# Optimization experiments

Hardware: AMD Instinct MI355X
Metric: run time of the kernel (lower is better)

## Reference

```python
import jax, jax.numpy as jnp
import numpy as np

DIM = 768
NUM_HEADS = 12
HIDDEN = int(DIM * 4.0)
EPS = 1e-5


def setup_inputs() -> dict:
    key = jax.random.key(0)
    ks = jax.random.split(key, 8)
    s = lambda k, shape, scale=0.02: jax.random.normal(k, shape, dtype=jnp.float32) * scale
    return {
        "x": jax.random.normal(ks[0], (8, 1024, DIM), dtype=jnp.float32),
        "ln1_g": jnp.ones((DIM,), jnp.float32),
        "ln1_b": jnp.zeros((DIM,), jnp.float32),
        "qkv_w": s(ks[1], (DIM, 3 * DIM)),
        "qkv_b": jnp.zeros((3 * DIM,), jnp.float32),
        "proj_w": s(ks[2], (DIM, DIM)),
        "proj_b": jnp.zeros((DIM,), jnp.float32),
        "ln2_g": jnp.ones((DIM,), jnp.float32),
        "ln2_b": jnp.zeros((DIM,), jnp.float32),
        "fc1_w": s(ks[3], (DIM, HIDDEN)),
        "fc1_b": jnp.zeros((HIDDEN,), jnp.float32),
        "fc2_w": s(ks[4], (HIDDEN, DIM)),
        "fc2_b": jnp.zeros((DIM,), jnp.float32),
    }


def layer_norm(x, g, b):
    mu = jnp.mean(x, axis=-1, keepdims=True)
    var = jnp.mean(jnp.square(x - mu), axis=-1, keepdims=True)
    return (x - mu) * jax.lax.rsqrt(var + EPS) * g + b


def reference(x, ln1_g, ln1_b, qkv_w, qkv_b, proj_w, proj_b,
              ln2_g, ln2_b, fc1_w, fc1_b, fc2_w, fc2_b):
    B, N, C = x.shape
    H = NUM_HEADS
    Dh = C // H
    scale = Dh ** -0.5

    # --- Attention (pre-norm) ---
    h = layer_norm(x, ln1_g, ln1_b)
    qkv = h @ qkv_w + qkv_b                       # [B, N, 3C]
    qkv = qkv.reshape(B, N, 3, H, Dh)
    q, k, v = qkv[:, :, 0], qkv[:, :, 1], qkv[:, :, 2]  # [B, N, H, Dh]
    attn = jnp.einsum("bqhd,bkhd->bhqk", q, k) * scale  # [B, H, N, N]
    attn = jax.nn.softmax(attn, axis=-1)
    o = jnp.einsum("bhqk,bkhd->bqhd", attn, v).reshape(B, N, C)
    x = x + (o @ proj_w + proj_b)

    # --- MLP (pre-norm) ---
    h = layer_norm(x, ln2_g, ln2_b)
    h = jax.nn.gelu(h @ fc1_w + fc1_b, approximate=False)  # torch nn.GELU = exact erf
    x = x + (h @ fc2_w + fc2_b)
    return x
```

## Files before the change

kernel.cpp:

```cpp
#include <hip/hip_runtime.h>
#include <hip/hip_bf16.h>
#include <cstdint>

using f32x4  = __attribute__((ext_vector_type(4))) float;
using bf16x8 = __attribute__((ext_vector_type(8))) short;

__device__ inline ushort f2bf(float f) {
    union { float f; uint u; } x; x.f = f;
    uint u = x.u;
    return (ushort)((u + 0x7FFFu + ((u >> 16) & 1u)) >> 16);
}

__device__ inline void unpack8(uint4 v, float* out) {
    uint ws[4] = {v.x, v.y, v.z, v.w};
#pragma unroll
    for (int i = 0; i < 4; ++i) {
        union { uint u; float f; } lo, hi;
        lo.u = ws[i] << 16;
        hi.u = ws[i] & 0xFFFF0000u;
        out[2 * i]     = lo.f;
        out[2 * i + 1] = hi.f;
    }
}

__device__ inline void gload16(const ushort* g, ushort* lds) {
    __builtin_amdgcn_global_load_lds(
        (const __attribute__((address_space(1))) unsigned int*)g,
        (__attribute__((address_space(3))) unsigned int*)lds, 16, 0, 0);
}

__global__ __launch_bounds__(256) void transpose_cast(const float* __restrict__ w,
                                                      ushort* __restrict__ wt,
                                                      int K, int N) {
    __shared__ float tile[32][33];
    const int bn = blockIdx.x * 32;
    const int bk = blockIdx.y * 32;
    const int tx = threadIdx.x & 31, ty = threadIdx.x >> 5;
#pragma unroll
    for (int i = 0; i < 32; i += 8)
        tile[ty + i][tx] = w[(size_t)(bk + ty + i) * N + bn + tx];
    __syncthreads();
#pragma unroll
    for (int i = 0; i < 32; i += 8)
        wt[(size_t)(bn + ty + i) * K + bk + tx] = f2bf(tile[tx][ty + i]);
}

__global__ __launch_bounds__(256) void ln_bf16(const float* __restrict__ x,
                                               const float* __restrict__ g,
                                               const float* __restrict__ b,
                                               ushort* __restrict__ out) {
    const int row = blockIdx.x;
    const float* xr = x + (size_t)row * 768;
    const int t = threadIdx.x;
    float v0 = xr[t], v1 = xr[t + 256], v2 = xr[t + 512];
    float s  = v0 + v1 + v2;
    float sq = v0 * v0 + v1 * v1 + v2 * v2;
#pragma unroll
    for (int off = 32; off > 0; off >>= 1) {
        s  += __shfl_down(s, off);
        sq += __shfl_down(sq, off);
    }
    __shared__ float sa[4], sb[4];
    const int wv = t >> 6, lane = t & 63;
    if (lane == 0) { sa[wv] = s; sb[wv] = sq; }
    __syncthreads();
    s  = sa[0] + sa[1] + sa[2] + sa[3];
    sq = sb[0] + sb[1] + sb[2] + sb[3];
    const float mu   = s * (1.0f / 768.0f);
    const float var  = sq * (1.0f / 768.0f) - mu * mu;
    const float rstd = rsqrtf(var + 1e-5f);
    ushort* orow = out + (size_t)row * 768;
    orow[t]       = f2bf((v0 - mu) * rstd * g[t]       + b[t]);
    orow[t + 256] = f2bf((v1 - mu) * rstd * g[t + 256] + b[t + 256]);
    orow[t + 512] = f2bf((v2 - mu) * rstd * g[t + 512] + b[t + 512]);
}

template <int EPI>
__global__ __launch_bounds__(256) void gemm_bt(const ushort* __restrict__ A,
                                               const ushort* __restrict__ Bt,
                                               const float* __restrict__ bias,
                                               const float* __restrict__ resid,
                                               void* __restrict__ out,
                                               int M, int N, int K) {
    __shared__ ushort As[128 * 32];
    __shared__ ushort Bs[128 * 32];
    const int t    = threadIdx.x;
    const int lane = t & 63;
    const int w    = t >> 6;
    const int wr   = w >> 1, wc = w & 1;
    const int bm   = blockIdx.y * 128, bn = blockIdx.x * 128;
    const int lr   = lane >> 4, lc = lane & 15;
    const int srow = lane >> 2;
    const int sk8  = (lane & 3) * 8;

    const f32x4 fzero = {0.f, 0.f, 0.f, 0.f};
    f32x4 acc[4][4];
#pragma unroll
    for (int ai = 0; ai < 4; ++ai)
#pragma unroll
        for (int bj = 0; bj < 4; ++bj) acc[ai][bj] = fzero;

    const ushort* Ag0 = A  + (size_t)(bm + w * 16 + srow) * K + sk8;
    const ushort* Ag1 = Ag0 + (size_t)64 * K;
    const ushort* Bg0 = Bt + (size_t)(bn + w * 16 + srow) * K + sk8;
    const ushort* Bg1 = Bg0 + (size_t)64 * K;
    ushort* lA0 = &As[(w * 16) * 32];
    ushort* lA1 = &As[(64 + w * 16) * 32];
    ushort* lB0 = &Bs[(w * 16) * 32];
    ushort* lB1 = &Bs[(64 + w * 16) * 32];

    for (int kb = 0; kb < K; kb += 32) {
        __syncthreads();
        gload16(Ag0 + kb, lA0);
        gload16(Ag1 + kb, lA1);
        gload16(Bg0 + kb, lB0);
        gload16(Bg1 + kb, lB1);
        __syncthreads();
        bf16x8 af[4], bf[4];
#pragma unroll
        for (int ai = 0; ai < 4; ++ai)
            af[ai] = *(const bf16x8*)&As[(wr * 64 + ai * 16 + lc) * 32 + lr * 8];
#pragma unroll
        for (int bj = 0; bj < 4; ++bj)
            bf[bj] = *(const bf16x8*)&Bs[(wc * 64 + bj * 16 + lc) * 32 + lr * 8];
#pragma unroll
        for (int ai = 0; ai < 4; ++ai)
#pragma unroll
            for (int bj = 0; bj < 4; ++bj)
                acc[ai][bj] = __builtin_amdgcn_mfma_f32_16x16x32_bf16(af[ai], bf[bj],
                                                                      acc[ai][bj], 0, 0, 0);
    }

#pragma unroll
    for (int ai = 0; ai < 4; ++ai) {
#pragma unroll
        for (int bj = 0; bj < 4; ++bj) {
            int col  = bn + wc * 64 + bj * 16 + lc;
            float bs = bias[col];
#pragma unroll
            for (int j = 0; j < 4; ++j) {
                int row   = bm + wr * 64 + ai * 16 + lr * 4 + j;
                float val = acc[ai][bj][j] + bs;
                if (EPI == 1) {
                    val += resid[(size_t)row * N + col];
                    ((float*)out)[(size_t)row * N + col] = val;
                } else if (EPI == 2) {
                    val = 0.5f * val * (1.0f + erff(val * 0.70710678118f));
                    ((ushort*)out)[(size_t)row * N + col] = f2bf(val);
                } else {
                    ((ushort*)out)[(size_t)row * N + col] = f2bf(val);
                }
            }
        }
    }
}

__global__ __launch_bounds__(256) void attn_mfma(const ushort* __restrict__ qkv,
                                                 ushort* __restrict__ outb) {
    __shared__ ushort Kls[64 * 72];
    __shared__ ushort Vtls[64 * 72];
    __shared__ ushort Pls[4][32 * 72];

    const int bid = blockIdx.x;
    const int b   = bid / 96;
    const int rem = bid % 96;
    const int h   = rem >> 3;
    const int qc  = rem & 7;
    const int t    = threadIdx.x;
    const int w    = t >> 6;
    const int lane = t & 63;
    const int lr   = lane >> 4, lc = lane & 15;
    const int q0   = qc * 128 + w * 32;
    const size_t bbase = (size_t)b * 1024;

    bf16x8 qa[2][2];
#pragma unroll
    for (int rt = 0; rt < 2; ++rt)
#pragma unroll
        for (int ds = 0; ds < 2; ++ds) {
            uint4 u = *(const uint4*)(qkv + (bbase + q0 + rt * 16 + lc) * 2304 +
                                      h * 64 + ds * 32 + lr * 8);
            float tmp[8];
            unpack8(u, tmp);
            bf16x8 v;
#pragma unroll
            for (int j = 0; j < 8; ++j) v[j] = (short)f2bf(tmp[j] * 0.125f);
            qa[rt][ds] = v;
        }

    const f32x4 fzero = {0.f, 0.f, 0.f, 0.f};
    f32x4 O[2][4];
    float m[2][4], l[2][4];
#pragma unroll
    for (int rt = 0; rt < 2; ++rt) {
#pragma unroll
        for (int dt = 0; dt < 4; ++dt) O[rt][dt] = fzero;
#pragma unroll
        for (int j = 0; j < 4; ++j) { m[rt][j] = -INFINITY; l[rt][j] = 0.0f; }
    }

    for (int kt = 0; kt < 16; ++kt) {
        const int k0 = kt * 64;
        __syncthreads();
#pragma unroll
        for (int i = 0; i < 2; ++i) {
            int idx = t + i * 256;
            int key = idx >> 3, seg = idx & 7;
            uint4 u = *(const uint4*)(qkv + (bbase + k0 + key) * 2304 + 768 +
                                      h * 64 + seg * 8);
            *(uint4*)&Kls[key * 72 + seg * 8] = u;
        }
        {
            int key = t & 63, dblk = t >> 6;
#pragma unroll
            for (int i = 0; i < 2; ++i) {
                int d0 = dblk * 8 + i * 32;
                uint4 u = *(const uint4*)(qkv + (bbase + k0 + key) * 2304 + 1536 +
                                          h * 64 + d0);
                const ushort* us = (const ushort*)&u;
#pragma unroll
                for (int j = 0; j < 8; ++j) Vtls[(d0 + j) * 72 + key] = us[j];
            }
        }
        __syncthreads();

        f32x4 s4[2][4];
#pragma unroll
        for (int rt = 0; rt < 2; ++rt)
#pragma unroll
            for (int kt4 = 0; kt4 < 4; ++kt4) {
                f32x4 acc = fzero;
#pragma unroll
                for (int ds = 0; ds < 2; ++ds) {
                    bf16x8 kb = *(const bf16x8*)&Kls[(kt4 * 16 + lc) * 72 + ds * 32 + lr * 8];
                    acc = __builtin_amdgcn_mfma_f32_16x16x32_bf16(qa[rt][ds], kb, acc, 0, 0, 0);
                }
                s4[rt][kt4] = acc;
            }

#pragma unroll
        for (int rt = 0; rt < 2; ++rt) {
#pragma unroll
            for (int j = 0; j < 4; ++j) {
                float v = fmaxf(fmaxf(s4[rt][0][j], s4[rt][1][j]),
                                fmaxf(s4[rt][2][j], s4[rt][3][j]));
#pragma unroll
                for (int off = 1; off < 16; off <<= 1) v = fmaxf(v, __shfl_xor(v, off));
                float mn = fmaxf(m[rt][j], v);
                float c  = __expf(m[rt][j] - mn);
                m[rt][j] = mn;
                float psum = 0.f;
#pragma unroll
                for (int kt4 = 0; kt4 < 4; ++kt4) {
                    float p = __expf(s4[rt][kt4][j] - mn);
                    s4[rt][kt4][j] = p;
                    psum += p;
                }
#pragma unroll
                for (int off = 1; off < 16; off <<= 1) psum += __shfl_xor(psum, off);
                l[rt][j] = l[rt][j] * c + psum;
#pragma unroll
                for (int dt = 0; dt < 4; ++dt) O[rt][dt][j] *= c;
                int prow = rt * 16 + lr * 4 + j;
#pragma unroll
                for (int kt4 = 0; kt4 < 4; ++kt4)
                    Pls[w][prow * 72 + kt4 * 16 + lc] = f2bf(s4[rt][kt4][j]);
            }
        }

        bf16x8 pa[2][2];
#pragma unroll
        for (int rt = 0; rt < 2; ++rt)
#pragma unroll
            for (int ks = 0; ks < 2; ++ks)
                pa[rt][ks] = *(const bf16x8*)&Pls[w][(rt * 16 + lc) * 72 + ks * 32 + lr * 8];
#pragma unroll
        for (int dt = 0; dt < 4; ++dt)
#pragma unroll
            for (int ks = 0; ks < 2; ++ks) {
                bf16x8 vb = *(const bf16x8*)&Vtls[(dt * 16 + lc) * 72 + ks * 32 + lr * 8];
#pragma unroll
                for (int rt = 0; rt < 2; ++rt)
                    O[rt][dt] = __builtin_amdgcn_mfma_f32_16x16x32_bf16(pa[rt][ks], vb,
                                                                        O[rt][dt], 0, 0, 0);
            }
    }

#pragma unroll
    for (int rt = 0; rt < 2; ++rt)
#pragma unroll
        for (int j = 0; j < 4; ++j) {
            float inv = 1.0f / l[rt][j];
            size_t row = bbase + q0 + rt * 16 + lr * 4 + j;
#pragma unroll
            for (int dt = 0; dt < 4; ++dt)
                outb[row * 768 + h * 64 + dt * 16 + lc] = f2bf(O[rt][dt][j] * inv);
        }
}

extern "C" void kernel_launch(void* const* d_in, const int* in_sizes, int n_in,
                              void* d_out, int out_size, void* d_ws, size_t ws_size,
                              hipStream_t stream) {
    const float* x      = (const float*)d_in[0];
    const float* ln1_g  = (const float*)d_in[1];
    const float* ln1_b  = (const float*)d_in[2];
    const float* qkv_w  = (const float*)d_in[3];
    const float* qkv_b  = (const float*)d_in[4];
    const float* proj_w = (const float*)d_in[5];
    const float* proj_b = (const float*)d_in[6];
    const float* ln2_g  = (const float*)d_in[7];
    const float* ln2_b  = (const float*)d_in[8];
    const float* fc1_w  = (const float*)d_in[9];
    const float* fc1_b  = (const float*)d_in[10];
    const float* fc2_w  = (const float*)d_in[11];
    const float* fc2_b  = (const float*)d_in[12];

    char* ws = (char*)d_ws;
    auto alloc = [&](size_t bytes) {
        char* p = ws;
        ws += (bytes + 255) & ~(size_t)255;
        return p;
    };
    ushort* qkv_wt  = (ushort*)alloc((size_t)768 * 2304 * 2);
    ushort* proj_wt = (ushort*)alloc((size_t)768 * 768 * 2);
    ushort* fc1_wt  = (ushort*)alloc((size_t)768 * 3072 * 2);
    ushort* fc2_wt  = (ushort*)alloc((size_t)3072 * 768 * 2);
    ushort* hb      = (ushort*)alloc((size_t)8192 * 768 * 2);
    ushort* qkvb    = (ushort*)alloc((size_t)8192 * 2304 * 2);
    ushort* ob      = (ushort*)alloc((size_t)8192 * 768 * 2);
    float*  x1      = (float*)alloc((size_t)8192 * 768 * 4);
    ushort* h2b     = (ushort*)alloc((size_t)8192 * 768 * 2);
    ushort* h3b     = (ushort*)alloc((size_t)8192 * 3072 * 2);

    transpose_cast<<<dim3(2304 / 32, 768 / 32), 256, 0, stream>>>(qkv_w, qkv_wt, 768, 2304);
    transpose_cast<<<dim3(768 / 32, 768 / 32), 256, 0, stream>>>(proj_w, proj_wt, 768, 768);
    transpose_cast<<<dim3(3072 / 32, 768 / 32), 256, 0, stream>>>(fc1_w, fc1_wt, 768, 3072);
    transpose_cast<<<dim3(768 / 32, 3072 / 32), 256, 0, stream>>>(fc2_w, fc2_wt, 3072, 768);

    ln_bf16<<<8192, 256, 0, stream>>>(x, ln1_g, ln1_b, hb);
    gemm_bt<0><<<dim3(2304 / 128, 8192 / 128), 256, 0, stream>>>(hb, qkv_wt, qkv_b, nullptr,
                                                                 qkvb, 8192, 2304, 768);
    attn_mfma<<<8 * 12 * 8, 256, 0, stream>>>(qkvb, ob);
    gemm_bt<1><<<dim3(768 / 128, 8192 / 128), 256, 0, stream>>>(ob, proj_wt, proj_b, x,
                                                                x1, 8192, 768, 768);
    ln_bf16<<<8192, 256, 0, stream>>>(x1, ln2_g, ln2_b, h2b);
    gemm_bt<2><<<dim3(3072 / 128, 8192 / 128), 256, 0, stream>>>(h2b, fc1_wt, fc1_b, nullptr,
                                                                 h3b, 8192, 3072, 768);
    gemm_bt<1><<<dim3(768 / 128, 8192 / 128), 256, 0, stream>>>(h3b, fc2_wt, fc2_b, x1,
                                                                (float*)d_out, 8192, 768, 3072);
}
```

Before: 347.6 us.

## Deepen GEMM K-tile, swizzle blocks across XCDs, prefetch K/V and lazily rescale attention

The GEMM now stages 64-wide K slices per barrier instead of 32, which halves the sync count, and launches a 1-D grid remapped so neighbouring tiles land on the same XCD for L2 reuse. The attention kernel gets the same XCD swizzle and prefetches the next K/V tile into registers while the current one is computed. It also uses exp2 with log2e folded into the Q scale and skips the O/l rescale unless the running max grows by more than 8. MFMA sections are wrapped in s_setprio. These changes cut barrier overhead and global load latency and add some register and LDS pressure. The lazy-rescale threshold accepts slightly larger intermediate values before a rescale.

```diff
diff --git a/kernel.cpp b/kernel.cpp
--- a/kernel.cpp
+++ b/kernel.cpp
@@ -27,6 +27,11 @@
     __builtin_amdgcn_global_load_lds(
         (const __attribute__((address_space(1))) unsigned int*)g,
         (__attribute__((address_space(3))) unsigned int*)lds, 16, 0, 0);
+}
+
+__device__ inline int xcd_swz(int bid, int nwg) {
+    int c = nwg >> 3;
+    return (bid & 7) * c + (bid >> 3);
 }
 
 __global__ __launch_bounds__(256) void transpose_cast(const float* __restrict__ w,
@@ -81,17 +86,16 @@
                                                const float* __restrict__ bias,
                                                const float* __restrict__ resid,
                                                void* __restrict__ out,
-                                               int M, int N, int K) {
-    __shared__ ushort As[128 * 32];
-    __shared__ ushort Bs[128 * 32];
+                                               int M, int N, int K, int gx) {
+    __shared__ ushort As[128 * 64];
+    __shared__ ushort Bs[128 * 64];
+    const int tile = xcd_swz(blockIdx.x, gridDim.x);
+    const int bm   = (tile / gx) * 128, bn = (tile % gx) * 128;
     const int t    = threadIdx.x;
     const int lane = t & 63;
     const int w    = t >> 6;
     const int wr   = w >> 1, wc = w & 1;
-    const int bm   = blockIdx.y * 128, bn = blockIdx.x * 128;
     const int lr   = lane >> 4, lc = lane & 15;
-    const int srow = lane >> 2;
-    const int sk8  = (lane & 3) * 8;
 
     const f32x4 fzero = {0.f, 0.f, 0.f, 0.f};
     f32x4 acc[4][4];
@@ -100,35 +104,44 @@
 #pragma unroll
         for (int bj = 0; bj < 4; ++bj) acc[ai][bj] = fzero;
 
-    const ushort* Ag0 = A  + (size_t)(bm + w * 16 + srow) * K + sk8;
-    const ushort* Ag1 = Ag0 + (size_t)64 * K;
-    const ushort* Bg0 = Bt + (size_t)(bn + w * 16 + srow) * K + sk8;
-    const ushort* Bg1 = Bg0 + (size_t)64 * K;
-    ushort* lA0 = &As[(w * 16) * 32];
-    ushort* lA1 = &As[(64 + w * 16) * 32];
-    ushort* lB0 = &Bs[(w * 16) * 32];
-    ushort* lB1 = &Bs[(64 + w * 16) * 32];
-
-    for (int kb = 0; kb < K; kb += 32) {
+    const int srow = lane >> 3, sk8 = (lane & 7) * 8;
+    const ushort* Ag[4];
+    const ushort* Bg[4];
+    ushort* lA[4];
+    ushort* lB[4];
+#pragma unroll
+    for (int i = 0; i < 4; ++i) {
+        int j = w * 4 + i;
+        Ag[i] = A  + (size_t)(bm + j * 8 + srow) * K + sk8;
+        Bg[i] = Bt + (size_t)(bn + j * 8 + srow) * K + sk8;
+        lA[i] = &As[j * 512];
+        lB[i] = &Bs[j * 512];
+    }
+
+    for (int kb = 0; kb < K; kb += 64) {
         __syncthreads();
-        gload16(Ag0 + kb, lA0);
-        gload16(Ag1 + kb, lA1);
-        gload16(Bg0 + kb, lB0);
-        gload16(Bg1 + kb, lB1);
+#pragma unroll
+        for (int i = 0; i < 4; ++i) {
+            gload16(Ag[i] + kb, lA[i]);
+            gload16(Bg[i] + kb, lB[i]);
+        }
         __syncthreads();
-        bf16x8 af[4], bf[4];
-#pragma unroll
-        for (int ai = 0; ai < 4; ++ai)
-            af[ai] = *(const bf16x8*)&As[(wr * 64 + ai * 16 + lc) * 32 + lr * 8];
-#pragma unroll
-        for (int bj = 0; bj < 4; ++bj)
-            bf[bj] = *(const bf16x8*)&Bs[(wc * 64 + bj * 16 + lc) * 32 + lr * 8];
-#pragma unroll
-        for (int ai = 0; ai < 4; ++ai)
+#pragma unroll
+        for (int ks = 0; ks < 2; ++ks) {
+            bf16x8 af[4], bf[4];
+#pragma unroll
+            for (int ai = 0; ai < 4; ++ai)
+                af[ai] = *(const bf16x8*)&As[(wr * 64 + ai * 16 + lc) * 64 + ks * 32 + lr * 8];
 #pragma unroll
             for (int bj = 0; bj < 4; ++bj)
-                acc[ai][bj] = __builtin_amdgcn_mfma_f32_16x16x32_bf16(af[ai], bf[bj],
-                                                                      acc[ai][bj], 0, 0, 0);
+                bf[bj] = *(const bf16x8*)&Bs[(wc * 64 + bj * 16 + lc) * 64 + ks * 32 + lr * 8];
+#pragma unroll
+            for (int ai = 0; ai < 4; ++ai)
+#pragma unroll
+                for (int bj = 0; bj < 4; ++bj)
+                    acc[ai][bj] = __builtin_amdgcn_mfma_f32_16x16x32_bf16(af[ai], bf[bj],
+                                                                          acc[ai][bj], 0, 0, 0);
+        }
     }
 
 #pragma unroll
@@ -161,9 +174,9 @@
     __shared__ ushort Vtls[64 * 72];
     __shared__ ushort Pls[4][32 * 72];
 
-    const int bid = blockIdx.x;
-    const int b   = bid / 96;
-    const int rem = bid % 96;
+    const int tile = xcd_swz(blockIdx.x, 768);
+    const int b   = tile / 96;
+    const int rem = tile % 96;
     const int h   = rem >> 3;
     const int qc  = rem & 7;
     const int t    = threadIdx.x;
@@ -173,6 +186,7 @@
     const int q0   = qc * 128 + w * 32;
     const size_t bbase = (size_t)b * 1024;
 
+    const float qscale = 0.125f * 1.44269504088896f;
     bf16x8 qa[2][2];
 #pragma unroll
     for (int rt = 0; rt < 2; ++rt)
@@ -184,7 +198,7 @@
             unpack8(u, tmp);
             bf16x8 v;
 #pragma unroll
-            for (int j = 0; j < 8; ++j) v[j] = (short)f2bf(tmp[j] * 0.125f);
+            for (int j = 0; j < 8; ++j) v[j] = (short)f2bf(tmp[j] * qscale);
             qa[rt][ds] = v;
         }
 
@@ -199,32 +213,37 @@
         for (int j = 0; j < 4; ++j) { m[rt][j] = -INFINITY; l[rt][j] = 0.0f; }
     }
 
+    const int kkey0 = t >> 3, kseg = (t & 7) * 8;
+    const int vkey  = t & 63, vdblk = t >> 6;
+    uint4 kreg0, kreg1, vreg0, vreg1;
+    auto issue_loads = [&](int k0) {
+        size_t kb0 = (bbase + k0 + kkey0) * 2304 + 768 + h * 64 + kseg;
+        kreg0 = *(const uint4*)(qkv + kb0);
+        kreg1 = *(const uint4*)(qkv + kb0 + (size_t)32 * 2304);
+        size_t vb0 = (bbase + k0 + vkey) * 2304 + 1536 + h * 64 + vdblk * 8;
+        vreg0 = *(const uint4*)(qkv + vb0);
+        vreg1 = *(const uint4*)(qkv + vb0 + 32);
+    };
+    issue_loads(0);
+
     for (int kt = 0; kt < 16; ++kt) {
-        const int k0 = kt * 64;
         __syncthreads();
-#pragma unroll
-        for (int i = 0; i < 2; ++i) {
-            int idx = t + i * 256;
-            int key = idx >> 3, seg = idx & 7;
-            uint4 u = *(const uint4*)(qkv + (bbase + k0 + key) * 2304 + 768 +
-                                      h * 64 + seg * 8);
-            *(uint4*)&Kls[key * 72 + seg * 8] = u;
-        }
+        *(uint4*)&Kls[kkey0 * 72 + kseg]        = kreg0;
+        *(uint4*)&Kls[(32 + kkey0) * 72 + kseg] = kreg1;
         {
-            int key = t & 63, dblk = t >> 6;
-#pragma unroll
-            for (int i = 0; i < 2; ++i) {
-                int d0 = dblk * 8 + i * 32;
-                uint4 u = *(const uint4*)(qkv + (bbase + k0 + key) * 2304 + 1536 +
-                                          h * 64 + d0);
-                const ushort* us = (const ushort*)&u;
-#pragma unroll
-                for (int j = 0; j < 8; ++j) Vtls[(d0 + j) * 72 + key] = us[j];
+            const ushort* u0 = (const ushort*)&vreg0;
+            const ushort* u1 = (const ushort*)&vreg1;
+#pragma unroll
+            for (int j = 0; j < 8; ++j) {
+                Vtls[(vdblk * 8 + j) * 72 + vkey]      = u0[j];
+                Vtls[(vdblk * 8 + 32 + j) * 72 + vkey] = u1[j];
             }
         }
         __syncthreads();
+        if (kt < 15) issue_loads((kt + 1) * 64);
 
         f32x4 s4[2][4];
+        __builtin_amdgcn_s_setprio(1);
 #pragma unroll
         for (int rt = 0; rt < 2; ++rt)
 #pragma unroll
@@ -237,6 +256,7 @@
                 }
                 s4[rt][kt4] = acc;
             }
+        __builtin_amdgcn_s_setprio(0);
 
 #pragma unroll
         for (int rt = 0; rt < 2; ++rt) {
@@ -246,25 +266,25 @@
                                 fmaxf(s4[rt][2][j], s4[rt][3][j]));
 #pragma unroll
                 for (int off = 1; off < 16; off <<= 1) v = fmaxf(v, __shfl_xor(v, off));
-                float mn = fmaxf(m[rt][j], v);
-                float c  = __expf(m[rt][j] - mn);
-                m[rt][j] = mn;
+                float mn = m[rt][j];
+                if (v > mn + 8.0f) {
+                    float c = exp2f(mn - v);
+                    mn = v; m[rt][j] = v;
+                    l[rt][j] *= c;
+#pragma unroll
+                    for (int dt = 0; dt < 4; ++dt) O[rt][dt][j] *= c;
+                }
                 float psum = 0.f;
+                int prow = rt * 16 + lr * 4 + j;
 #pragma unroll
                 for (int kt4 = 0; kt4 < 4; ++kt4) {
-                    float p = __expf(s4[rt][kt4][j] - mn);
-                    s4[rt][kt4][j] = p;
+                    float p = exp2f(s4[rt][kt4][j] - mn);
                     psum += p;
+                    Pls[w][prow * 72 + kt4 * 16 + lc] = f2bf(p);
                 }
 #pragma unroll
                 for (int off = 1; off < 16; off <<= 1) psum += __shfl_xor(psum, off);
-                l[rt][j] = l[rt][j] * c + psum;
-#pragma unroll
-                for (int dt = 0; dt < 4; ++dt) O[rt][dt][j] *= c;
-                int prow = rt * 16 + lr * 4 + j;
-#pragma unroll
-                for (int kt4 = 0; kt4 < 4; ++kt4)
-                    Pls[w][prow * 72 + kt4 * 16 + lc] = f2bf(s4[rt][kt4][j]);
+                l[rt][j] += psum;
             }
         }
 
@@ -274,6 +294,7 @@
 #pragma unroll
             for (int ks = 0; ks < 2; ++ks)
                 pa[rt][ks] = *(const bf16x8*)&Pls[w][(rt * 16 + lc) * 72 + ks * 32 + lr * 8];
+        __builtin_amdgcn_s_setprio(1);
 #pragma unroll
         for (int dt = 0; dt < 4; ++dt)
 #pragma unroll
@@ -284,6 +305,7 @@
                     O[rt][dt] = __builtin_amdgcn_mfma_f32_16x16x32_bf16(pa[rt][ks], vb,
                                                                         O[rt][dt], 0, 0, 0);
             }
+        __builtin_amdgcn_s_setprio(0);
     }
 
 #pragma unroll
@@ -338,14 +360,14 @@
     transpose_cast<<<dim3(768 / 32, 3072 / 32), 256, 0, stream>>>(fc2_w, fc2_wt, 3072, 768);
 
     ln_bf16<<<8192, 256, 0, stream>>>(x, ln1_g, ln1_b, hb);
-    gemm_bt<0><<<dim3(2304 / 128, 8192 / 128), 256, 0, stream>>>(hb, qkv_wt, qkv_b, nullptr,
-                                                                 qkvb, 8192, 2304, 768);
-    attn_mfma<<<8 * 12 * 8, 256, 0, stream>>>(qkvb, ob);
-    gemm_bt<1><<<dim3(768 / 128, 8192 / 128), 256, 0, stream>>>(ob, proj_wt, proj_b, x,
-                                                                x1, 8192, 768, 768);
+    gemm_bt<0><<<18 * 64, 256, 0, stream>>>(hb, qkv_wt, qkv_b, nullptr,
+                                            qkvb, 8192, 2304, 768, 18);
+    attn_mfma<<<768, 256, 0, stream>>>(qkvb, ob);
+    gemm_bt<1><<<6 * 64, 256, 0, stream>>>(ob, proj_wt, proj_b, x,
+                                           x1, 8192, 768, 768, 6);
     ln_bf16<<<8192, 256, 0, stream>>>(x1, ln2_g, ln2_b, h2b);
-    gemm_bt<2><<<dim3(3072 / 128, 8192 / 128), 256, 0, stream>>>(h2b, fc1_wt, fc1_b, nullptr,
-                                                                 h3b, 8192, 3072, 768);
-    gemm_bt<1><<<dim3(768 / 128, 8192 / 128), 256, 0, stream>>>(h3b, fc2_wt, fc2_b, x1,
-                                                                (float*)d_out, 8192, 768, 3072);
-}
+    gemm_bt<2><<<24 * 64, 256, 0, stream>>>(h2b, fc1_wt, fc1_b, nullptr,
+                                            h3b, 8192, 3072, 768, 24);
+    gemm_bt<1><<<6 * 64, 256, 0, stream>>>(h3b, fc2_wt, fc2_b, x1,
+                                           (float*)d_out, 8192, 768, 3072, 6);
+}
```

After: 387.2 us. 11.4% more time.
